# Optimization experiments

Hardware: AMD Instinct MI355X
Metric: run time of the kernel (lower is better)

Reference implementation:

```python
import jax, jax.numpy as jnp
from jax import lax
import numpy as np

B = 16
E, NH, FF, L = 768, 12, 3072, 8
D = E // NH  # 64, per-head dim
PATCH_DIM = 16 * 16 * 16  # 4096


def setup_inputs() -> dict:
    key = jax.random.key(0)
    ks = jax.random.split(key, 16)
    s = 0.02
    def n(k, shape):
        return jax.random.normal(k, shape, dtype=jnp.float32) * s
    return {
        "x": jax.random.normal(ks[0], (B, 512, 512, 3), dtype=jnp.float32),
        "conv1_w": n(ks[1], (3, 3, 3, 16)), "conv1_b": jnp.zeros((16,), jnp.float32),
        "conv2_w": n(ks[2], (3, 3, 16, 16)), "conv2_b": jnp.zeros((16,), jnp.float32),
        "proj_w": n(ks[3], (PATCH_DIM, E)), "proj_b": jnp.zeros((E,), jnp.float32),
        "Wq": n(ks[4], (L, E, E)), "bq": jnp.zeros((L, E), jnp.float32),
        "Wk": n(ks[5], (L, E, E)), "bk": jnp.zeros((L, E), jnp.float32),
        "Wv": n(ks[6], (L, E, E)), "bv": jnp.zeros((L, E), jnp.float32),
        "Wo": n(ks[7], (L, E, E)), "bo": jnp.zeros((L, E), jnp.float32),
        "W1": n(ks[8], (L, E, FF)), "b1": jnp.zeros((L, FF), jnp.float32),
        "W2": n(ks[9], (L, FF, E)), "b2": jnp.zeros((L, E), jnp.float32),
        "ln1_g": jnp.ones((L, E), jnp.float32), "ln1_b": jnp.zeros((L, E), jnp.float32),
        "ln2_g": jnp.ones((L, E), jnp.float32), "ln2_b": jnp.zeros((L, E), jnp.float32),
        "head_w": n(ks[10], (E, 1)), "head_b": jnp.zeros((1,), jnp.float32),
    }


def _ln(x, g, b, eps=1e-6):
    m = jnp.mean(x, axis=-1, keepdims=True)
    v = jnp.var(x, axis=-1, keepdims=True)
    return (x - m) * lax.rsqrt(v + eps) * g + b


def _forward(x, conv1_w, conv1_b, conv2_w, conv2_b, proj_w, proj_b,
             Wq, bq, Wk, bk, Wv, bv, Wo, bo, W1, b1, W2, b2,
             ln1_g, ln1_b, ln2_g, ln2_b, head_w, head_b):
    dn = ('NHWC', 'HWIO', 'NHWC')
    h = jax.nn.relu(lax.conv_general_dilated(x, conv1_w, (1, 1), 'VALID', dimension_numbers=dn) + conv1_b)
    h = lax.reduce_window(h, -jnp.inf, lax.max, (1, 2, 2, 1), (1, 2, 2, 1), 'VALID')  # (B,255,255,16)
    h = jax.nn.relu(lax.conv_general_dilated(h, conv2_w, (1, 1), 'VALID', dimension_numbers=dn) + conv2_b)
    h = lax.reduce_window(h, -jnp.inf, lax.max, (1, 2, 2, 1), (1, 2, 2, 1), 'VALID')  # (B,126,126,16)
    # tf.image.extract_patches 16x16 stride 16 SAME: pad 126 -> 128 (1 before, 1 after)
    h = jnp.pad(h, ((0, 0), (1, 1), (1, 1), (0, 0)))
    Bc = h.shape[0]
    patches = h.reshape(Bc, 8, 16, 8, 16, 16).transpose(0, 1, 3, 2, 4, 5).reshape(Bc, 64, PATCH_DIM)
    t = patches @ proj_w + proj_b  # (B,64,768)
    scale = 1.0 / jnp.sqrt(jnp.float32(D))  # tf code scales by sqrt(per-head key dim)
    for i in range(L):
        q = (t @ Wq[i] + bq[i]).reshape(Bc, -1, NH, D).transpose(0, 2, 1, 3)
        k = (t @ Wk[i] + bk[i]).reshape(Bc, -1, NH, D).transpose(0, 2, 1, 3)
        v = (t @ Wv[i] + bv[i]).reshape(Bc, -1, NH, D).transpose(0, 2, 1, 3)
        w = jax.nn.softmax(jnp.einsum('bhqd,bhkd->bhqk', q, k) * scale, axis=-1)
        a = jnp.einsum('bhqk,bhkd->bhqd', w, v)  # (B,H,S,D)
        # FAITHFUL to original: reshape (B,H,S,D) -> (B,S,E) directly (no transpose back)
        a = a.reshape(Bc, -1, E)
        a = a @ Wo[i] + bo[i]
        o1 = _ln(t + a, ln1_g[i], ln1_b[i])
        f = jax.nn.relu(o1 @ W1[i] + b1[i]) @ W2[i] + b2[i]
        t = _ln(o1 + f, ln2_g[i], ln2_b[i])
    pooled = jnp.mean(t, axis=1)  # GlobalAveragePooling1D
    return jax.nn.sigmoid(pooled @ head_w + head_b)


def reference(x, conv1_w, conv1_b, conv2_w, conv2_b, proj_w, proj_b,
              Wq, bq, Wk, bk, Wv, bv, Wo, bo, W1, b1, W2, b2,
              ln1_g, ln1_b, ln2_g, ln2_b, head_w, head_b):
    return _forward(x, conv1_w, conv1_b, conv2_w, conv2_b, proj_w, proj_b,
                    Wq, bq, Wk, bk, Wv, bv, Wo, bo, W1, b1, W2, b2,
                    ln1_g, ln1_b, ln2_g, ln2_b, head_w, head_b)
```

## Files before the change

### kernel.cpp

```cpp
#include <hip/hip_runtime.h>
#include <hip/hip_bf16.h>
#include <cstdint>
#include <cstddef>

typedef __bf16 bf16;
typedef __attribute__((ext_vector_type(8))) __bf16 bf16x8;
typedef __attribute__((ext_vector_type(4))) float f32x4;

__global__ __launch_bounds__(256) void wtrans(const float* __restrict__ src,
    bf16* __restrict__ dst, int K, int N) {
  __shared__ float tile[32][33];
  int l = blockIdx.z;
  src += (size_t)l * K * N; dst += (size_t)l * K * N;
  int n0 = blockIdx.x * 32, k0 = blockIdx.y * 32;
  int tx = threadIdx.x & 31, ty = threadIdx.x >> 5;
#pragma unroll
  for (int i = 0; i < 4; i++) {
    int k = ty + i * 8;
    tile[k][tx] = src[(size_t)(k0 + k) * N + n0 + tx];
  }
  __syncthreads();
#pragma unroll
  for (int i = 0; i < 4; i++) {
    int n = ty + i * 8;
    dst[(size_t)(n0 + n) * K + k0 + tx] = (bf16)tile[tx][n];
  }
}

__global__ __launch_bounds__(256) void conv1_pool(const float* __restrict__ x,
    const float* __restrict__ w, const float* __restrict__ bias,
    bf16* __restrict__ out) {
  __shared__ float ws[432];
  __shared__ float bs[16];
  int t = threadIdx.x;
  for (int i = t; i < 432; i += 256) ws[i] = w[i];
  if (t < 16) bs[t] = bias[t];
  __syncthreads();
  int idx = blockIdx.x * 256 + t;
  if (idx >= 16 * 255 * 255) return;
  int xo = idx % 255; int tmp = idx / 255; int yo = tmp % 255; int b = tmp / 255;
  float best[16];
#pragma unroll
  for (int c = 0; c < 16; c++) best[c] = 0.f;
#pragma unroll
  for (int py = 0; py < 2; py++)
#pragma unroll
  for (int px = 0; px < 2; px++) {
    float acc[16];
#pragma unroll
    for (int c = 0; c < 16; c++) acc[c] = bs[c];
    int iy0 = yo * 2 + py, ix0 = xo * 2 + px;
    for (int ky = 0; ky < 3; ky++)
    for (int kx = 0; kx < 3; kx++) {
      const float* xp = x + ((size_t)(b * 512 + iy0 + ky) * 512 + (ix0 + kx)) * 3;
      float v0 = xp[0], v1 = xp[1], v2 = xp[2];
      const float* wp = &ws[((ky * 3 + kx) * 3) * 16];
#pragma unroll
      for (int c = 0; c < 16; c++) acc[c] = fmaf(v0, wp[c], acc[c]);
#pragma unroll
      for (int c = 0; c < 16; c++) acc[c] = fmaf(v1, wp[16 + c], acc[c]);
#pragma unroll
      for (int c = 0; c < 16; c++) acc[c] = fmaf(v2, wp[32 + c], acc[c]);
    }
#pragma unroll
    for (int c = 0; c < 16; c++) best[c] = fmaxf(best[c], acc[c]);
  }
  bf16* op = out + (size_t)idx * 16;
#pragma unroll
  for (int c = 0; c < 16; c++) op[c] = (bf16)best[c];
}

#define C2STR 20
__global__ __launch_bounds__(256) void conv2_pool_patch(const bf16* __restrict__ in,
    const float* __restrict__ w, const float* __restrict__ bias,
    bf16* __restrict__ patches) {
  __shared__ bf16 xs[34 * 34 * C2STR];
  __shared__ float ws[2304];
  __shared__ float bs[16];
  int t = threadIdx.x;
  int tx = blockIdx.x, ty = blockIdx.y, b = blockIdx.z;
  for (int i = t; i < 2304; i += 256) ws[i] = w[i];
  if (t < 16) bs[t] = bias[t];
  int r0 = 32 * ty - 2, c0 = 32 * tx - 2;
  for (int i = t; i < 1156; i += 256) {
    int rr = i / 34, cc = i % 34;
    int gr = min(max(r0 + rr, 0), 254), gc = min(max(c0 + cc, 0), 254);
    const bf16* ip = in + ((size_t)(b * 255 + gr) * 255 + gc) * 16;
    uint4 v0 = *(const uint4*)ip;
    uint4 v1 = *(const uint4*)(ip + 8);
    bf16* op = &xs[i * C2STR];
    *(uint4*)op = v0;
    *(uint4*)(op + 8) = v1;
  }
  __syncthreads();
  int py_ = t >> 4, px_ = t & 15;
  int yp = ty * 16 + py_, xp = tx * 16 + px_;
  bf16* op = patches + ((size_t)(b * 64 + ty * 8 + tx) * 4096 + py_ * 256 + px_ * 16);
  if (yp == 0 || yp == 127 || xp == 0 || xp == 127) {
#pragma unroll
    for (int c = 0; c < 16; c++) op[c] = (bf16)0.f;
    return;
  }
  float best[16];
#pragma unroll
  for (int c = 0; c < 16; c++) best[c] = 0.f;
  for (int py = 0; py < 2; py++)
  for (int px = 0; px < 2; px++) {
    float acc[16];
#pragma unroll
    for (int c = 0; c < 16; c++) acc[c] = bs[c];
    for (int ky = 0; ky < 3; ky++)
    for (int kx = 0; kx < 3; kx++) {
      int lr_ = 2 * py_ + py + ky, lc_ = 2 * px_ + px + kx;
      const bf16* xpp = &xs[(lr_ * 34 + lc_) * C2STR];
      const float* wp = &ws[(ky * 3 + kx) * 256];
#pragma unroll
      for (int ci = 0; ci < 16; ci++) {
        float v = (float)xpp[ci];
#pragma unroll
        for (int c = 0; c < 16; c++) acc[c] = fmaf(v, wp[ci * 16 + c], acc[c]);
      }
    }
#pragma unroll
    for (int c = 0; c < 16; c++) best[c] = fmaxf(best[c], acc[c]);
  }
#pragma unroll
  for (int c = 0; c < 16; c++) op[c] = (bf16)best[c];
}

#define LSTR 72

template<int MODE>
__device__ __forceinline__ void gemm_core(const bf16* __restrict__ A,
    const bf16* __restrict__ Bt, const float* __restrict__ bias,
    float* __restrict__ Cf, bf16* __restrict__ Cb,
    int bm, int bn, int N, int K, int k0, int kc) {
  __shared__ alignas(16) bf16 As[64 * LSTR];
  __shared__ alignas(16) bf16 Bs[64 * LSTR];
  int t = threadIdx.x, lane = t & 63, wave = t >> 6;
  int wm = (wave >> 1) * 32, wn = (wave & 1) * 32;
  int lq = lane >> 4, lr = lane & 15;
  f32x4 acc[2][2];
#pragma unroll
  for (int i = 0; i < 2; i++)
#pragma unroll
  for (int j = 0; j < 2; j++) acc[i][j] = (f32x4){0.f, 0.f, 0.f, 0.f};
  int r = t >> 2, c = (t & 3) * 16;
  const bf16* Ap = A + (size_t)(bm + r) * K + k0 + c;
  const bf16* Bp = Bt + (size_t)(bn + r) * K + k0 + c;
  bf16* AsW = &As[r * LSTR + c];
  bf16* BsW = &Bs[r * LSTR + c];
  uint4 a0 = *(const uint4*)Ap, a1 = *(const uint4*)(Ap + 8);
  uint4 b0 = *(const uint4*)Bp, b1 = *(const uint4*)(Bp + 8);
  for (int kk = 64; kk <= kc; kk += 64) {
    *(uint4*)AsW = a0; *(uint4*)(AsW + 8) = a1;
    *(uint4*)BsW = b0; *(uint4*)(BsW + 8) = b1;
    __syncthreads();
    if (kk < kc) {
      Ap += 64; Bp += 64;
      a0 = *(const uint4*)Ap; a1 = *(const uint4*)(Ap + 8);
      b0 = *(const uint4*)Bp; b1 = *(const uint4*)(Bp + 8);
    }
#pragma unroll
    for (int ks = 0; ks < 2; ks++) {
      bf16x8 af0 = *(const bf16x8*)&As[(wm + lr) * LSTR + ks * 32 + lq * 8];
      bf16x8 af1 = *(const bf16x8*)&As[(wm + 16 + lr) * LSTR + ks * 32 + lq * 8];
      bf16x8 bfr0 = *(const bf16x8*)&Bs[(wn + lr) * LSTR + ks * 32 + lq * 8];
      bf16x8 bfr1 = *(const bf16x8*)&Bs[(wn + 16 + lr) * LSTR + ks * 32 + lq * 8];
      acc[0][0] = __builtin_amdgcn_mfma_f32_16x16x32_bf16(af0, bfr0, acc[0][0], 0, 0, 0);
      acc[0][1] = __builtin_amdgcn_mfma_f32_16x16x32_bf16(af0, bfr1, acc[0][1], 0, 0, 0);
      acc[1][0] = __builtin_amdgcn_mfma_f32_16x16x32_bf16(af1, bfr0, acc[1][0], 0, 0, 0);
      acc[1][1] = __builtin_amdgcn_mfma_f32_16x16x32_bf16(af1, bfr1, acc[1][1], 0, 0, 0);
    }
    __syncthreads();
  }
#pragma unroll
  for (int mi = 0; mi < 2; mi++)
#pragma unroll
  for (int ni = 0; ni < 2; ni++) {
    int col = bn + wn + ni * 16 + lr;
#pragma unroll
    for (int rr = 0; rr < 4; rr++) {
      int row = bm + wm + mi * 16 + lq * 4 + rr;
      float v = acc[mi][ni][rr];
      if (MODE == 1) {
        v = fmaxf(v + bias[col], 0.f);
        Cb[(size_t)row * N + col] = (bf16)v;
      } else {
        Cf[(size_t)row * N + col] = v;
      }
    }
  }
}

template<int MODE>
__global__ __launch_bounds__(256) void gemm_std(const bf16* __restrict__ A,
    const bf16* __restrict__ Bt, const float* __restrict__ bias,
    float* __restrict__ Cf, bf16* __restrict__ Cb, int N, int K, int KC) {
  int s = blockIdx.z;
  float* Cfp = Cf ? Cf + (size_t)s * 1024 * N : nullptr;
  gemm_core<MODE>(A, Bt, bias, Cfp, Cb, blockIdx.y * 64, blockIdx.x * 64, N, K, s * KC, KC);
}

__global__ __launch_bounds__(256) void gemm_qkv(const bf16* __restrict__ A,
    const bf16* __restrict__ Btq, const bf16* __restrict__ Btk, const bf16* __restrict__ Btv,
    float* __restrict__ qp, float* __restrict__ kp, float* __restrict__ vp) {
  int z = blockIdx.z;
  int sel = z >> 1, s = z & 1;
  const bf16* Bt = (sel == 0) ? Btq : (sel == 1) ? Btk : Btv;
  float* C = ((sel == 0) ? qp : (sel == 1) ? kp : vp) + (size_t)s * 786432;
  gemm_core<0>(A, Bt, nullptr, C, nullptr, blockIdx.y * 64, blockIdx.x * 64, 768, 768, s * 384, 384);
}

__global__ __launch_bounds__(256) void attn_kernel(const float* __restrict__ Qp,
    const float* __restrict__ Kp, const float* __restrict__ Vp,
    const float* __restrict__ bq, const float* __restrict__ bk, const float* __restrict__ bv,
    bf16* __restrict__ Aout) {
  __shared__ alignas(16) float qs[64 * 68];
  __shared__ alignas(16) float ks[64 * 68];
  __shared__ alignas(16) float ss[64 * 68];
  int t = threadIdx.x;
  int bh = blockIdx.x; int b = bh / 12, h = bh % 12;
  size_t base = (size_t)b * 49152 + h * 64;
  const float* qb0 = Qp + base; const float* qb1 = qb0 + 786432;
  const float* kb0 = Kp + base; const float* kb1 = kb0 + 786432;
  const float* vb0 = Vp + base; const float* vb1 = vb0 + 786432;
  {
    int s = t >> 2, qd = (t & 3) * 16;
#pragma unroll
    for (int j = 0; j < 16; j += 4) {
      float4 q0 = *(const float4*)(qb0 + (size_t)s * 768 + qd + j);
      float4 q1 = *(const float4*)(qb1 + (size_t)s * 768 + qd + j);
      float4 qb4 = *(const float4*)(bq + h * 64 + qd + j);
      float4 k0 = *(const float4*)(kb0 + (size_t)s * 768 + qd + j);
      float4 k1 = *(const float4*)(kb1 + (size_t)s * 768 + qd + j);
      float4 kb4 = *(const float4*)(bk + h * 64 + qd + j);
      qs[s * 68 + qd + j + 0] = q0.x + q1.x + qb4.x;
      qs[s * 68 + qd + j + 1] = q0.y + q1.y + qb4.y;
      qs[s * 68 + qd + j + 2] = q0.z + q1.z + qb4.z;
      qs[s * 68 + qd + j + 3] = q0.w + q1.w + qb4.w;
      ks[s * 68 + qd + j + 0] = k0.x + k1.x + kb4.x;
      ks[s * 68 + qd + j + 1] = k0.y + k1.y + kb4.y;
      ks[s * 68 + qd + j + 2] = k0.z + k1.z + kb4.z;
      ks[s * 68 + qd + j + 3] = k0.w + k1.w + kb4.w;
    }
  }
  __syncthreads();
  int r = t >> 4, c = t & 15;
  {
    float sc[4][4];
#pragma unroll
    for (int i = 0; i < 4; i++)
#pragma unroll
    for (int j = 0; j < 4; j++) sc[i][j] = 0.f;
    for (int k = 0; k < 64; k += 4) {
      float4 qv[4], kv[4];
#pragma unroll
      for (int i = 0; i < 4; i++) qv[i] = *(const float4*)&qs[(r + 16 * i) * 68 + k];
#pragma unroll
      for (int j = 0; j < 4; j++) kv[j] = *(const float4*)&ks[(c + 16 * j) * 68 + k];
#pragma unroll
      for (int i = 0; i < 4; i++)
#pragma unroll
      for (int j = 0; j < 4; j++)
        sc[i][j] += qv[i].x * kv[j].x + qv[i].y * kv[j].y + qv[i].z * kv[j].z + qv[i].w * kv[j].w;
    }
#pragma unroll
    for (int i = 0; i < 4; i++)
#pragma unroll
    for (int j = 0; j < 4; j++)
      ss[(r + 16 * i) * 68 + c + 16 * j] = sc[i][j] * 0.125f;
  }
  __syncthreads();
  {
    int d = t & 63, s0 = (t >> 6) * 16;
    float bvd = bv[h * 64 + d];
    alignas(16) float vv[16];
#pragma unroll
    for (int i = 0; i < 16; i++)
      vv[i] = vb0[(size_t)(s0 + i) * 768 + d] + vb1[(size_t)(s0 + i) * 768 + d] + bvd;
#pragma unroll
    for (int i = 0; i < 16; i += 4) *(float4*)&qs[d * 68 + s0 + i] = *(float4*)&vv[i];
  }
  {
    int lane = t & 63, wave = t >> 6;
    for (int rr = 0; rr < 16; rr++) {
      int row = wave * 16 + rr;
      float v = ss[row * 68 + lane];
      float m = v;
#pragma unroll
      for (int off = 32; off > 0; off >>= 1) m = fmaxf(m, __shfl_xor(m, off));
      float e = __expf(v - m);
      float ssum = e;
#pragma unroll
      for (int off = 32; off > 0; off >>= 1) ssum += __shfl_xor(ssum, off);
      ss[row * 68 + lane] = e / ssum;
    }
  }
  __syncthreads();
  {
    float oc[4][4];
#pragma unroll
    for (int i = 0; i < 4; i++)
#pragma unroll
    for (int j = 0; j < 4; j++) oc[i][j] = 0.f;
    for (int k = 0; k < 64; k += 4) {
      float4 pv[4], vv[4];
#pragma unroll
      for (int i = 0; i < 4; i++) pv[i] = *(const float4*)&ss[(r + 16 * i) * 68 + k];
#pragma unroll
      for (int j = 0; j < 4; j++) vv[j] = *(const float4*)&qs[(c + 16 * j) * 68 + k];
#pragma unroll
      for (int i = 0; i < 4; i++)
#pragma unroll
      for (int j = 0; j < 4; j++)
        oc[i][j] += pv[i].x * vv[j].x + pv[i].y * vv[j].y + pv[i].z * vv[j].z + pv[i].w * vv[j].w;
    }
    bf16* ob = Aout + (size_t)b * 49152 + h * 4096;
#pragma unroll
    for (int i = 0; i < 4; i++)
#pragma unroll
    for (int j = 0; j < 4; j++)
      ob[(r + 16 * i) * 64 + c + 16 * j] = (bf16)oc[i][j];
  }
}

template<int S>
__global__ __launch_bounds__(256) void ln_kernel(const float* __restrict__ X,
    const float* __restrict__ Y, const float* __restrict__ yb,
    const float* __restrict__ g, const float* __restrict__ bta,
    float* __restrict__ Of, bf16* __restrict__ Ob) {
  int row = blockIdx.x, t = threadIdx.x;
  const float* xp = X + (size_t)row * 768;
  float vals[3]; float s = 0.f, s2 = 0.f;
#pragma unroll
  for (int i = 0; i < 3; i++) {
    int e = t + 256 * i;
    float v = xp[e] + yb[e];
#pragma unroll
    for (int p = 0; p < S; p++) v += Y[(size_t)p * 786432 + (size_t)row * 768 + e];
    vals[i] = v; s += v; s2 = fmaf(v, v, s2);
  }
#pragma unroll
  for (int off = 32; off > 0; off >>= 1) { s += __shfl_xor(s, off); s2 += __shfl_xor(s2, off); }
  __shared__ float rs[4], rs2[4];
  if ((t & 63) == 0) { rs[t >> 6] = s; rs2[t >> 6] = s2; }
  __syncthreads();
  s = rs[0] + rs[1] + rs[2] + rs[3];
  s2 = rs2[0] + rs2[1] + rs2[2] + rs2[3];
  float mean = s * (1.f / 768.f);
  float var = s2 * (1.f / 768.f) - mean * mean;
  float rstd = rsqrtf(var + 1e-6f);
  float* ofp = Of + (size_t)row * 768;
  bf16* obp = Ob + (size_t)row * 768;
#pragma unroll
  for (int i = 0; i < 3; i++) {
    int e = t + 256 * i;
    float o = (vals[i] - mean) * rstd * g[e] + bta[e];
    ofp[e] = o; obp[e] = (bf16)o;
  }
}

__global__ __launch_bounds__(256) void reduce2(const float* __restrict__ P,
    const float* __restrict__ bias, float* __restrict__ Of, bf16* __restrict__ Ob) {
  int row = blockIdx.x, t = threadIdx.x;
#pragma unroll
  for (int i = 0; i < 3; i++) {
    int e = t + 256 * i;
    float v = P[(size_t)row * 768 + e] + P[786432 + (size_t)row * 768 + e] + bias[e];
    Of[(size_t)row * 768 + e] = v;
    Ob[(size_t)row * 768 + e] = (bf16)v;
  }
}

__global__ __launch_bounds__(256) void head_kernel(const float* __restrict__ T,
    const float* __restrict__ hw, const float* __restrict__ hbp, float* __restrict__ out) {
  int b = blockIdx.x, t = threadIdx.x;
  float acc = 0.f;
#pragma unroll
  for (int i = 0; i < 3; i++) {
    int e = t + 256 * i;
    float s = 0.f;
    for (int si = 0; si < 64; si++) s += T[(size_t)(b * 64 + si) * 768 + e];
    acc = fmaf(s * (1.f / 64.f), hw[e], acc);
  }
#pragma unroll
  for (int off = 32; off > 0; off >>= 1) acc += __shfl_xor(acc, off);
  __shared__ float rs[4];
  if ((t & 63) == 0) rs[t >> 6] = acc;
  __syncthreads();
  if (t == 0) {
    float z = rs[0] + rs[1] + rs[2] + rs[3] + hbp[0];
    out[b] = 1.f / (1.f + expf(-z));
  }
}

extern "C" void kernel_launch(void* const* d_in, const int* in_sizes, int n_in,
                              void* d_out, int out_size, void* d_ws, size_t ws_size,
                              hipStream_t stream) {
  const float* x     = (const float*)d_in[0];
  const float* c1w   = (const float*)d_in[1];
  const float* c1b   = (const float*)d_in[2];
  const float* c2w   = (const float*)d_in[3];
  const float* c2b   = (const float*)d_in[4];
  const float* projw = (const float*)d_in[5];
  const float* projb = (const float*)d_in[6];
  const float* Wq    = (const float*)d_in[7];
  const float* bq    = (const float*)d_in[8];
  const float* Wk    = (const float*)d_in[9];
  const float* bk    = (const float*)d_in[10];
  const float* Wv    = (const float*)d_in[11];
  const float* bv    = (const float*)d_in[12];
  const float* Wo    = (const float*)d_in[13];
  const float* bo    = (const float*)d_in[14];
  const float* W1    = (const float*)d_in[15];
  const float* b1    = (const float*)d_in[16];
  const float* W2    = (const float*)d_in[17];
  const float* b2    = (const float*)d_in[18];
  const float* ln1g  = (const float*)d_in[19];
  const float* ln1b  = (const float*)d_in[20];
  const float* ln2g  = (const float*)d_in[21];
  const float* ln2b  = (const float*)d_in[22];
  const float* headw = (const float*)d_in[23];
  const float* headb = (const float*)d_in[24];
  float* out = (float*)d_out;

  char* wp = (char*)d_ws;
  auto alloc = [&](size_t bytes) { char* p = wp; wp += (bytes + 255) & ~(size_t)255; return p; };
  bf16* c1p     = (bf16*)alloc((size_t)16 * 255 * 255 * 16 * 2);
  bf16* patches = (bf16*)alloc((size_t)1024 * 4096 * 2);
  bf16* projT   = (bf16*)alloc((size_t)4096 * 768 * 2);
  bf16* WqT     = (bf16*)alloc((size_t)8 * 768 * 768 * 2);
  bf16* WkT     = (bf16*)alloc((size_t)8 * 768 * 768 * 2);
  bf16* WvT     = (bf16*)alloc((size_t)8 * 768 * 768 * 2);
  bf16* WoT     = (bf16*)alloc((size_t)8 * 768 * 768 * 2);
  bf16* W1T     = (bf16*)alloc((size_t)8 * 768 * 3072 * 2);
  bf16* W2T     = (bf16*)alloc((size_t)8 * 3072 * 768 * 2);
  float* pp     = (float*)alloc((size_t)2 * 1024 * 768 * 4);
  float* tf     = (float*)alloc((size_t)1024 * 768 * 4);
  bf16*  tb     = (bf16*)alloc((size_t)1024 * 768 * 2);
  float* qp     = (float*)alloc((size_t)2 * 1024 * 768 * 4);
  float* kp     = (float*)alloc((size_t)2 * 1024 * 768 * 4);
  float* vp     = (float*)alloc((size_t)2 * 1024 * 768 * 4);
  float* wop    = (float*)alloc((size_t)2 * 1024 * 768 * 4);
  float* w2p    = (float*)alloc((size_t)4 * 1024 * 768 * 4);
  bf16*  ab     = (bf16*)alloc((size_t)1024 * 768 * 2);
  float* o1f    = (float*)alloc((size_t)1024 * 768 * 4);
  bf16*  o1b    = (bf16*)alloc((size_t)1024 * 768 * 2);
  bf16*  hbuf   = (bf16*)alloc((size_t)1024 * 3072 * 2);

  wtrans<<<dim3(24, 128, 1), 256, 0, stream>>>(projw, projT, 4096, 768);
  wtrans<<<dim3(24, 24, 8), 256, 0, stream>>>(Wq, WqT, 768, 768);
  wtrans<<<dim3(24, 24, 8), 256, 0, stream>>>(Wk, WkT, 768, 768);
  wtrans<<<dim3(24, 24, 8), 256, 0, stream>>>(Wv, WvT, 768, 768);
  wtrans<<<dim3(24, 24, 8), 256, 0, stream>>>(Wo, WoT, 768, 768);
  wtrans<<<dim3(96, 24, 8), 256, 0, stream>>>(W1, W1T, 768, 3072);
  wtrans<<<dim3(24, 96, 8), 256, 0, stream>>>(W2, W2T, 3072, 768);

  conv1_pool<<<4065, 256, 0, stream>>>(x, c1w, c1b, c1p);
  conv2_pool_patch<<<dim3(8, 8, 16), 256, 0, stream>>>(c1p, c2w, c2b, patches);
  gemm_std<0><<<dim3(12, 16, 2), 256, 0, stream>>>(patches, projT, nullptr, pp, nullptr, 768, 4096, 2048);
  reduce2<<<1024, 256, 0, stream>>>(pp, projb, tf, tb);

  for (int i = 0; i < 8; i++) {
    gemm_qkv<<<dim3(12, 16, 6), 256, 0, stream>>>(tb,
        WqT + (size_t)i * 589824, WkT + (size_t)i * 589824, WvT + (size_t)i * 589824,
        qp, kp, vp);
    attn_kernel<<<192, 256, 0, stream>>>(qp, kp, vp,
        bq + i * 768, bk + i * 768, bv + i * 768, ab);
    gemm_std<0><<<dim3(12, 16, 2), 256, 0, stream>>>(ab, WoT + (size_t)i * 589824,
        nullptr, wop, nullptr, 768, 768, 384);
    ln_kernel<2><<<1024, 256, 0, stream>>>(tf, wop, bo + i * 768,
        ln1g + i * 768, ln1b + i * 768, o1f, o1b);
    gemm_std<1><<<dim3(48, 16, 1), 256, 0, stream>>>(o1b, W1T + (size_t)i * 2359296,
        b1 + i * 3072, nullptr, hbuf, 3072, 768, 768);
    gemm_std<0><<<dim3(12, 16, 4), 256, 0, stream>>>(hbuf, W2T + (size_t)i * 2359296,
        nullptr, w2p, nullptr, 768, 3072, 768);
    ln_kernel<4><<<1024, 256, 0, stream>>>(o1f, w2p, b2 + i * 768,
        ln2g + i * 768, ln2b + i * 768, tf, tb);
  }
  head_kernel<<<16, 256, 0, stream>>>(tf, headw, headb, out);
}
```

Baseline: 1.132 ms.

## Replace GEMMs with 128x128 swizzled direct-to-LDS tiles, fuse QKV weights, vectorize conv2

All GEMMs now use a new 128x128-tile kernel. It loads global memory straight into LDS with global_load_lds, uses an XOR-swizzled layout instead of padding, and gives each wave a 4x4 grid of MFMA tiles. Q, K and V weights are packed into one 2304-wide matrix so a single GEMM produces all three. Split-K factors are retuned and one partial buffer is shared across stages, with a templated reduction. Conv2 reads its channels from LDS as packed words and converts bf16 by bit shifts. The larger tiles cut LDS traffic per MFMA but reduce grid size. The loop is single-buffered with no prefetch overlap, which may expose load latency.

Measured after the change: 1.308 ms. +15.5%, slower.

```diff
diff --git a/kernel.cpp b/kernel.cpp
--- a/kernel.cpp
+++ b/kernel.cpp
@@ -7,11 +7,18 @@
 typedef __attribute__((ext_vector_type(8))) __bf16 bf16x8;
 typedef __attribute__((ext_vector_type(4))) float f32x4;
 
+__device__ __forceinline__ void gl_lds16(const bf16* g, bf16* l) {
+  __builtin_amdgcn_global_load_lds((const __attribute__((address_space(1))) void*)g,
+                                   (__attribute__((address_space(3))) void*)l, 16, 0, 0);
+}
+__device__ __forceinline__ float bflo(unsigned u) { u <<= 16; return __builtin_bit_cast(float, u); }
+__device__ __forceinline__ float bfhi(unsigned u) { u &= 0xffff0000u; return __builtin_bit_cast(float, u); }
+
 __global__ __launch_bounds__(256) void wtrans(const float* __restrict__ src,
-    bf16* __restrict__ dst, int K, int N) {
+    bf16* __restrict__ dst, int K, int N, size_t sls, size_t dls) {
   __shared__ float tile[32][33];
   int l = blockIdx.z;
-  src += (size_t)l * K * N; dst += (size_t)l * K * N;
+  src += (size_t)l * sls; dst += (size_t)l * dls;
   int n0 = blockIdx.x * 32, k0 = blockIdx.y * 32;
   int tx = threadIdx.x & 31, ty = threadIdx.x >> 5;
 #pragma unroll
@@ -70,7 +77,7 @@
   for (int c = 0; c < 16; c++) op[c] = (bf16)best[c];
 }
 
-#define C2STR 20
+#define C2STR 16
 __global__ __launch_bounds__(256) void conv2_pool_patch(const bf16* __restrict__ in,
     const float* __restrict__ w, const float* __restrict__ bias,
     bf16* __restrict__ patches) {
@@ -112,13 +119,17 @@
     for (int ky = 0; ky < 3; ky++)
     for (int kx = 0; kx < 3; kx++) {
       int lr_ = 2 * py_ + py + ky, lc_ = 2 * px_ + px + kx;
-      const bf16* xpp = &xs[(lr_ * 34 + lc_) * C2STR];
+      const uint2* xpp = (const uint2*)&xs[(lr_ * 34 + lc_) * C2STR];
+      uint2 w0 = xpp[0], w1 = xpp[1], w2 = xpp[2], w3 = xpp[3];
+      float v[16] = {bflo(w0.x), bfhi(w0.x), bflo(w0.y), bfhi(w0.y),
+                     bflo(w1.x), bfhi(w1.x), bflo(w1.y), bfhi(w1.y),
+                     bflo(w2.x), bfhi(w2.x), bflo(w2.y), bfhi(w2.y),
+                     bflo(w3.x), bfhi(w3.x), bflo(w3.y), bfhi(w3.y)};
       const float* wp = &ws[(ky * 3 + kx) * 256];
 #pragma unroll
       for (int ci = 0; ci < 16; ci++) {
-        float v = (float)xpp[ci];
-#pragma unroll
-        for (int c = 0; c < 16; c++) acc[c] = fmaf(v, wp[ci * 16 + c], acc[c]);
+#pragma unroll
+        for (int c = 0; c < 16; c++) acc[c] = fmaf(v[ci], wp[ci * 16 + c], acc[c]);
       }
     }
 #pragma unroll
@@ -128,92 +139,90 @@
   for (int c = 0; c < 16; c++) op[c] = (bf16)best[c];
 }
 
-#define LSTR 72
-
 template<int MODE>
-__device__ __forceinline__ void gemm_core(const bf16* __restrict__ A,
-    const bf16* __restrict__ Bt, const float* __restrict__ bias,
-    float* __restrict__ Cf, bf16* __restrict__ Cb,
-    int bm, int bn, int N, int K, int k0, int kc) {
-  __shared__ alignas(16) bf16 As[64 * LSTR];
-  __shared__ alignas(16) bf16 Bs[64 * LSTR];
-  int t = threadIdx.x, lane = t & 63, wave = t >> 6;
-  int wm = (wave >> 1) * 32, wn = (wave & 1) * 32;
-  int lq = lane >> 4, lr = lane & 15;
-  f32x4 acc[2][2];
-#pragma unroll
-  for (int i = 0; i < 2; i++)
-#pragma unroll
-  for (int j = 0; j < 2; j++) acc[i][j] = (f32x4){0.f, 0.f, 0.f, 0.f};
-  int r = t >> 2, c = (t & 3) * 16;
-  const bf16* Ap = A + (size_t)(bm + r) * K + k0 + c;
-  const bf16* Bp = Bt + (size_t)(bn + r) * K + k0 + c;
-  bf16* AsW = &As[r * LSTR + c];
-  bf16* BsW = &Bs[r * LSTR + c];
-  uint4 a0 = *(const uint4*)Ap, a1 = *(const uint4*)(Ap + 8);
-  uint4 b0 = *(const uint4*)Bp, b1 = *(const uint4*)(Bp + 8);
-  for (int kk = 64; kk <= kc; kk += 64) {
-    *(uint4*)AsW = a0; *(uint4*)(AsW + 8) = a1;
-    *(uint4*)BsW = b0; *(uint4*)(BsW + 8) = b1;
-    __syncthreads();
-    if (kk < kc) {
-      Ap += 64; Bp += 64;
-      a0 = *(const uint4*)Ap; a1 = *(const uint4*)(Ap + 8);
-      b0 = *(const uint4*)Bp; b1 = *(const uint4*)(Bp + 8);
-    }
-#pragma unroll
-    for (int ks = 0; ks < 2; ks++) {
-      bf16x8 af0 = *(const bf16x8*)&As[(wm + lr) * LSTR + ks * 32 + lq * 8];
-      bf16x8 af1 = *(const bf16x8*)&As[(wm + 16 + lr) * LSTR + ks * 32 + lq * 8];
-      bf16x8 bfr0 = *(const bf16x8*)&Bs[(wn + lr) * LSTR + ks * 32 + lq * 8];
-      bf16x8 bfr1 = *(const bf16x8*)&Bs[(wn + 16 + lr) * LSTR + ks * 32 + lq * 8];
-      acc[0][0] = __builtin_amdgcn_mfma_f32_16x16x32_bf16(af0, bfr0, acc[0][0], 0, 0, 0);
-      acc[0][1] = __builtin_amdgcn_mfma_f32_16x16x32_bf16(af0, bfr1, acc[0][1], 0, 0, 0);
-      acc[1][0] = __builtin_amdgcn_mfma_f32_16x16x32_bf16(af1, bfr0, acc[1][0], 0, 0, 0);
-      acc[1][1] = __builtin_amdgcn_mfma_f32_16x16x32_bf16(af1, bfr1, acc[1][1], 0, 0, 0);
-    }
-    __syncthreads();
-  }
-#pragma unroll
-  for (int mi = 0; mi < 2; mi++)
-#pragma unroll
-  for (int ni = 0; ni < 2; ni++) {
-    int col = bn + wn + ni * 16 + lr;
-#pragma unroll
-    for (int rr = 0; rr < 4; rr++) {
-      int row = bm + wm + mi * 16 + lq * 4 + rr;
-      float v = acc[mi][ni][rr];
-      if (MODE == 1) {
-        v = fmaxf(v + bias[col], 0.f);
-        Cb[(size_t)row * N + col] = (bf16)v;
-      } else {
-        Cf[(size_t)row * N + col] = v;
-      }
-    }
-  }
-}
-
-template<int MODE>
-__global__ __launch_bounds__(256) void gemm_std(const bf16* __restrict__ A,
+__global__ __launch_bounds__(256) void gemm128(const bf16* __restrict__ A,
     const bf16* __restrict__ Bt, const float* __restrict__ bias,
     float* __restrict__ Cf, bf16* __restrict__ Cb, int N, int K, int KC) {
+  __shared__ bf16 As[8192];
+  __shared__ bf16 Bs[8192];
   int s = blockIdx.z;
-  float* Cfp = Cf ? Cf + (size_t)s * 1024 * N : nullptr;
-  gemm_core<MODE>(A, Bt, bias, Cfp, Cb, blockIdx.y * 64, blockIdx.x * 64, N, K, s * KC, KC);
-}
-
-__global__ __launch_bounds__(256) void gemm_qkv(const bf16* __restrict__ A,
-    const bf16* __restrict__ Btq, const bf16* __restrict__ Btk, const bf16* __restrict__ Btv,
-    float* __restrict__ qp, float* __restrict__ kp, float* __restrict__ vp) {
-  int z = blockIdx.z;
-  int sel = z >> 1, s = z & 1;
-  const bf16* Bt = (sel == 0) ? Btq : (sel == 1) ? Btk : Btv;
-  float* C = ((sel == 0) ? qp : (sel == 1) ? kp : vp) + (size_t)s * 786432;
-  gemm_core<0>(A, Bt, nullptr, C, nullptr, blockIdx.y * 64, blockIdx.x * 64, 768, 768, s * 384, 384);
-}
-
-__global__ __launch_bounds__(256) void attn_kernel(const float* __restrict__ Qp,
-    const float* __restrict__ Kp, const float* __restrict__ Vp,
+  int bm = blockIdx.y * 128, bn = blockIdx.x * 128;
+  int t = threadIdx.x, lane = t & 63, wave = t >> 6;
+  int wm = (wave >> 1) * 64, wn = (wave & 1) * 64;
+  int lq = lane >> 4, lr = lane & 15;
+  f32x4 acc[4][4];
+#pragma unroll
+  for (int i = 0; i < 4; i++)
+#pragma unroll
+  for (int j = 0; j < 4; j++) acc[i][j] = (f32x4){0.f, 0.f, 0.f, 0.f};
+
+  int srow = wave * 32 + (lane >> 3);
+  int sch = (lane & 7) ^ (lane >> 3);
+  const bf16* Ag = A + (size_t)(bm + srow) * K + s * KC + sch * 8;
+  const bf16* Bg = Bt + (size_t)(bn + srow) * K + s * KC + sch * 8;
+  bf16* AsW = &As[wave * 2048];
+  bf16* BsW = &Bs[wave * 2048];
+
+  int key = lr & 7;
+  int aoff0 = ((lq ^ key) * 8);
+  int aoff1 = (((4 + lq) ^ key) * 8);
+
+  for (int kk = 0; kk < KC; kk += 64) {
+    gl_lds16(Ag, AsW);               gl_lds16(Ag + 8 * (size_t)K, AsW + 512);
+    gl_lds16(Ag + 16 * (size_t)K, AsW + 1024); gl_lds16(Ag + 24 * (size_t)K, AsW + 1536);
+    gl_lds16(Bg, BsW);               gl_lds16(Bg + 8 * (size_t)K, BsW + 512);
+    gl_lds16(Bg + 16 * (size_t)K, BsW + 1024); gl_lds16(Bg + 24 * (size_t)K, BsW + 1536);
+    Ag += 64; Bg += 64;
+    __syncthreads();
+#pragma unroll
+    for (int ks = 0; ks < 2; ks++) {
+      int ao = ks ? aoff1 : aoff0;
+      bf16x8 af[4], bfr[4];
+#pragma unroll
+      for (int i = 0; i < 4; i++) af[i] = *(const bf16x8*)&As[(wm + i * 16 + lr) * 64 + ao];
+#pragma unroll
+      for (int j = 0; j < 4; j++) bfr[j] = *(const bf16x8*)&Bs[(wn + j * 16 + lr) * 64 + ao];
+#pragma unroll
+      for (int i = 0; i < 4; i++)
+#pragma unroll
+      for (int j = 0; j < 4; j++)
+        acc[i][j] = __builtin_amdgcn_mfma_f32_16x16x32_bf16(af[i], bfr[j], acc[i][j], 0, 0, 0);
+    }
+    __syncthreads();
+  }
+
+  if (MODE == 0) {
+    float* Cp = Cf + (size_t)s * 1024 * N;
+#pragma unroll
+    for (int i = 0; i < 4; i++)
+#pragma unroll
+    for (int j = 0; j < 4; j++) {
+      int col = bn + wn + j * 16 + lr;
+      int row0 = bm + wm + i * 16 + lq * 4;
+#pragma unroll
+      for (int r = 0; r < 4; r++)
+        Cp[(size_t)(row0 + r) * N + col] = acc[i][j][r];
+    }
+  } else {
+#pragma unroll
+    for (int i = 0; i < 4; i++)
+#pragma unroll
+    for (int j = 0; j < 4; j++) {
+      int col = bn + wn + j * 16 + lr;
+      float bb = bias[col];
+      int row0 = bm + wm + i * 16 + lq * 4;
+#pragma unroll
+      for (int r = 0; r < 4; r++) {
+        float v = fmaxf(acc[i][j][r] + bb, 0.f);
+        Cb[(size_t)(row0 + r) * N + col] = (bf16)v;
+      }
+    }
+  }
+}
+
+#define QKVN 2304
+#define QKVP 2359296
+__global__ __launch_bounds__(256) void attn_kernel(const float* __restrict__ QKV,
     const float* __restrict__ bq, const float* __restrict__ bk, const float* __restrict__ bv,
     bf16* __restrict__ Aout) {
   __shared__ alignas(16) float qs[64 * 68];
@@ -221,28 +230,28 @@
   __shared__ alignas(16) float ss[64 * 68];
   int t = threadIdx.x;
   int bh = blockIdx.x; int b = bh / 12, h = bh % 12;
-  size_t base = (size_t)b * 49152 + h * 64;
-  const float* qb0 = Qp + base; const float* qb1 = qb0 + 786432;
-  const float* kb0 = Kp + base; const float* kb1 = kb0 + 786432;
-  const float* vb0 = Vp + base; const float* vb1 = vb0 + 786432;
+  size_t rb = (size_t)(b * 64) * QKVN;
+  const float* q0 = QKV + rb + h * 64;
+  const float* k0 = QKV + rb + 768 + h * 64;
+  const float* v0 = QKV + rb + 1536 + h * 64;
   {
     int s = t >> 2, qd = (t & 3) * 16;
 #pragma unroll
     for (int j = 0; j < 16; j += 4) {
-      float4 q0 = *(const float4*)(qb0 + (size_t)s * 768 + qd + j);
-      float4 q1 = *(const float4*)(qb1 + (size_t)s * 768 + qd + j);
+      float4 qa = *(const float4*)(q0 + (size_t)s * QKVN + qd + j);
+      float4 qb2 = *(const float4*)(q0 + QKVP + (size_t)s * QKVN + qd + j);
       float4 qb4 = *(const float4*)(bq + h * 64 + qd + j);
-      float4 k0 = *(const float4*)(kb0 + (size_t)s * 768 + qd + j);
-      float4 k1 = *(const float4*)(kb1 + (size_t)s * 768 + qd + j);
+      float4 ka = *(const float4*)(k0 + (size_t)s * QKVN + qd + j);
+      float4 kb2 = *(const float4*)(k0 + QKVP + (size_t)s * QKVN + qd + j);
       float4 kb4 = *(const float4*)(bk + h * 64 + qd + j);
-      qs[s * 68 + qd + j + 0] = q0.x + q1.x + qb4.x;
-      qs[s * 68 + qd + j + 1] = q0.y + q1.y + qb4.y;
-      qs[s * 68 + qd + j + 2] = q0.z + q1.z + qb4.z;
-      qs[s * 68 + qd + j + 3] = q0.w + q1.w + qb4.w;
-      ks[s * 68 + qd + j + 0] = k0.x + k1.x + kb4.x;
-      ks[s * 68 + qd + j + 1] = k0.y + k1.y + kb4.y;
-      ks[s * 68 + qd + j + 2] = k0.z + k1.z + kb4.z;
-      ks[s * 68 + qd + j + 3] = k0.w + k1.w + kb4.w;
+      qs[s * 68 + qd + j + 0] = qa.x + qb2.x + qb4.x;
+      qs[s * 68 + qd + j + 1] = qa.y + qb2.y + qb4.y;
+      qs[s * 68 + qd + j + 2] = qa.z + qb2.z + qb4.z;
+      qs[s * 68 + qd + j + 3] = qa.w + qb2.w + qb4.w;
+      ks[s * 68 + qd + j + 0] = ka.x + kb2.x + kb4.x;
+      ks[s * 68 + qd + j + 1] = ka.y + kb2.y + kb4.y;
+      ks[s * 68 + qd + j + 2] = ka.z + kb2.z + kb4.z;
+      ks[s * 68 + qd + j + 3] = ka.w + kb2.w + kb4.w;
     }
   }
   __syncthreads();
@@ -278,7 +287,7 @@
     alignas(16) float vv[16];
 #pragma unroll
     for (int i = 0; i < 16; i++)
-      vv[i] = vb0[(size_t)(s0 + i) * 768 + d] + vb1[(size_t)(s0 + i) * 768 + d] + bvd;
+      vv[i] = v0[(size_t)(s0 + i) * QKVN + d] + v0[QKVP + (size_t)(s0 + i) * QKVN + d] + bvd;
 #pragma unroll
     for (int i = 0; i < 16; i += 4) *(float4*)&qs[d * 68 + s0 + i] = *(float4*)&vv[i];
   }
@@ -361,13 +370,16 @@
   }
 }
 
-__global__ __launch_bounds__(256) void reduce2(const float* __restrict__ P,
+template<int S>
+__global__ __launch_bounds__(256) void reduceN(const float* __restrict__ P,
     const float* __restrict__ bias, float* __restrict__ Of, bf16* __restrict__ Ob) {
   int row = blockIdx.x, t = threadIdx.x;
 #pragma unroll
   for (int i = 0; i < 3; i++) {
     int e = t + 256 * i;
-    float v = P[(size_t)row * 768 + e] + P[786432 + (size_t)row * 768 + e] + bias[e];
+    float v = bias[e];
+#pragma unroll
+    for (int p = 0; p < S; p++) v += P[(size_t)p * 786432 + (size_t)row * 768 + e];
     Of[(size_t)row * 768 + e] = v;
     Ob[(size_t)row * 768 + e] = (bf16)v;
   }
@@ -430,53 +442,44 @@
   bf16* c1p     = (bf16*)alloc((size_t)16 * 255 * 255 * 16 * 2);
   bf16* patches = (bf16*)alloc((size_t)1024 * 4096 * 2);
   bf16* projT   = (bf16*)alloc((size_t)4096 * 768 * 2);
-  bf16* WqT     = (bf16*)alloc((size_t)8 * 768 * 768 * 2);
-  bf16* WkT     = (bf16*)alloc((size_t)8 * 768 * 768 * 2);
-  bf16* WvT     = (bf16*)alloc((size_t)8 * 768 * 768 * 2);
+  bf16* WqkvT   = (bf16*)alloc((size_t)8 * 2304 * 768 * 2);
   bf16* WoT     = (bf16*)alloc((size_t)8 * 768 * 768 * 2);
   bf16* W1T     = (bf16*)alloc((size_t)8 * 768 * 3072 * 2);
   bf16* W2T     = (bf16*)alloc((size_t)8 * 3072 * 768 * 2);
-  float* pp     = (float*)alloc((size_t)2 * 1024 * 768 * 4);
+  float* pbuf   = (float*)alloc((size_t)2 * 1024 * 2304 * 4);
   float* tf     = (float*)alloc((size_t)1024 * 768 * 4);
   bf16*  tb     = (bf16*)alloc((size_t)1024 * 768 * 2);
-  float* qp     = (float*)alloc((size_t)2 * 1024 * 768 * 4);
-  float* kp     = (float*)alloc((size_t)2 * 1024 * 768 * 4);
-  float* vp     = (float*)alloc((size_t)2 * 1024 * 768 * 4);
-  float* wop    = (float*)alloc((size_t)2 * 1024 * 768 * 4);
-  float* w2p    = (float*)alloc((size_t)4 * 1024 * 768 * 4);
   bf16*  ab     = (bf16*)alloc((size_t)1024 * 768 * 2);
   float* o1f    = (float*)alloc((size_t)1024 * 768 * 4);
   bf16*  o1b    = (bf16*)alloc((size_t)1024 * 768 * 2);
   bf16*  hbuf   = (bf16*)alloc((size_t)1024 * 3072 * 2);
 
-  wtrans<<<dim3(24, 128, 1), 256, 0, stream>>>(projw, projT, 4096, 768);
-  wtrans<<<dim3(24, 24, 8), 256, 0, stream>>>(Wq, WqT, 768, 768);
-  wtrans<<<dim3(24, 24, 8), 256, 0, stream>>>(Wk, WkT, 768, 768);
-  wtrans<<<dim3(24, 24, 8), 256, 0, stream>>>(Wv, WvT, 768, 768);
-  wtrans<<<dim3(24, 24, 8), 256, 0, stream>>>(Wo, WoT, 768, 768);
-  wtrans<<<dim3(96, 24, 8), 256, 0, stream>>>(W1, W1T, 768, 3072);
-  wtrans<<<dim3(24, 96, 8), 256, 0, stream>>>(W2, W2T, 3072, 768);
+  wtrans<<<dim3(24, 128, 1), 256, 0, stream>>>(projw, projT, 4096, 768, 0, 0);
+  wtrans<<<dim3(24, 24, 8), 256, 0, stream>>>(Wq, WqkvT,          768, 768, 589824, 1769472);
+  wtrans<<<dim3(24, 24, 8), 256, 0, stream>>>(Wk, WqkvT + 589824, 768, 768, 589824, 1769472);
+  wtrans<<<dim3(24, 24, 8), 256, 0, stream>>>(Wv, WqkvT + 1179648, 768, 768, 589824, 1769472);
+  wtrans<<<dim3(24, 24, 8), 256, 0, stream>>>(Wo, WoT, 768, 768, 589824, 589824);
+  wtrans<<<dim3(96, 24, 8), 256, 0, stream>>>(W1, W1T, 768, 3072, 2359296, 2359296);
+  wtrans<<<dim3(24, 96, 8), 256, 0, stream>>>(W2, W2T, 3072, 768, 2359296, 2359296);
 
   conv1_pool<<<4065, 256, 0, stream>>>(x, c1w, c1b, c1p);
   conv2_pool_patch<<<dim3(8, 8, 16), 256, 0, stream>>>(c1p, c2w, c2b, patches);
-  gemm_std<0><<<dim3(12, 16, 2), 256, 0, stream>>>(patches, projT, nullptr, pp, nullptr, 768, 4096, 2048);
-  reduce2<<<1024, 256, 0, stream>>>(pp, projb, tf, tb);
+  gemm128<0><<<dim3(6, 8, 4), 256, 0, stream>>>(patches, projT, nullptr, pbuf, nullptr, 768, 4096, 1024);
+  reduceN<4><<<1024, 256, 0, stream>>>(pbuf, projb, tf, tb);
 
   for (int i = 0; i < 8; i++) {
-    gemm_qkv<<<dim3(12, 16, 6), 256, 0, stream>>>(tb,
-        WqT + (size_t)i * 589824, WkT + (size_t)i * 589824, WvT + (size_t)i * 589824,
-        qp, kp, vp);
-    attn_kernel<<<192, 256, 0, stream>>>(qp, kp, vp,
-        bq + i * 768, bk + i * 768, bv + i * 768, ab);
-    gemm_std<0><<<dim3(12, 16, 2), 256, 0, stream>>>(ab, WoT + (size_t)i * 589824,
-        nullptr, wop, nullptr, 768, 768, 384);
-    ln_kernel<2><<<1024, 256, 0, stream>>>(tf, wop, bo + i * 768,
+    gemm128<0><<<dim3(18, 8, 2), 256, 0, stream>>>(tb, WqkvT + (size_t)i * 1769472,
+        nullptr, pbuf, nullptr, 2304, 768, 384);
+    attn_kernel<<<192, 256, 0, stream>>>(pbuf, bq + i * 768, bk + i * 768, bv + i * 768, ab);
+    gemm128<0><<<dim3(6, 8, 4), 256, 0, stream>>>(ab, WoT + (size_t)i * 589824,
+        nullptr, pbuf, nullptr, 768, 768, 192);
+    ln_kernel<4><<<1024, 256, 0, stream>>>(tf, pbuf, bo + i * 768,
         ln1g + i * 768, ln1b + i * 768, o1f, o1b);
-    gemm_std<1><<<dim3(48, 16, 1), 256, 0, stream>>>(o1b, W1T + (size_t)i * 2359296,
+    gemm128<1><<<dim3(24, 8, 1), 256, 0, stream>>>(o1b, W1T + (size_t)i * 2359296,
         b1 + i * 3072, nullptr, hbuf, 3072, 768, 768);
-    gemm_std<0><<<dim3(12, 16, 4), 256, 0, stream>>>(hbuf, W2T + (size_t)i * 2359296,
-        nullptr, w2p, nullptr, 768, 3072, 768);
-    ln_kernel<4><<<1024, 256, 0, stream>>>(o1f, w2p, b2 + i * 768,
+    gemm128<0><<<dim3(6, 8, 4), 256, 0, stream>>>(hbuf, W2T + (size_t)i * 2359296,
+        nullptr, pbuf, nullptr, 768, 3072, 768);
+    ln_kernel<4><<<1024, 256, 0, stream>>>(o1f, pbuf, b2 + i * 768,
         ln2g + i * 768, ln2b + i * 768, tf, tb);
   }
   head_kernel<<<16, 256, 0, stream>>>(tf, headw, headb, out);
```
